# Kernel tuning notes

Hardware: AMD Instinct MI355X
Metric: run time of the kernel (lower is better)

Reference implementation:

```python
import jax, jax.numpy as jnp
import numpy as np

N = 50000
E = 1600000
IN_CH = 128
OUT_CH = 128
NEG_SLOPE = 0.2


def _gat_conv(x, W, att_src, att_dst, bias, src, dst, heads, out_ch, concat):
    # x: [N, F_in], W: [F_in, heads*out_ch], att_*: [heads, out_ch]
    n = x.shape[0]
    h = (x @ W).reshape(n, heads, out_ch)                    # [N, H, C]
    a_src = jnp.einsum('nhc,hc->nh', h, att_src)             # [N, H]
    a_dst = jnp.einsum('nhc,hc->nh', h, att_dst)             # [N, H]
    logits = jax.nn.leaky_relu(a_src[src] + a_dst[dst], NEG_SLOPE)  # [Etot, H]
    m = jax.ops.segment_max(logits, dst, num_segments=n)     # per-dst max (self-loops ensure non-empty)
    e = jnp.exp(logits - m[dst])
    denom = jax.ops.segment_sum(e, dst, num_segments=n)
    alpha = e / denom[dst]                                   # [Etot, H]
    msgs = h[src] * alpha[:, :, None]                        # [Etot, H, C]
    out = jax.ops.segment_sum(msgs, dst, num_segments=n)     # [N, H, C]
    out = out.reshape(n, heads * out_ch) if concat else out.mean(axis=1)
    return out + bias


def setup_inputs() -> dict:
    key = jax.random.key(0)
    ks = jax.random.split(key, 12)
    x = jax.random.normal(ks[0], (N, IN_CH), dtype=jnp.float32)
    edge_index = jax.random.randint(ks[1], (2, E), 0, N, dtype=jnp.int32)
    s = 0.1
    W_map = jax.random.normal(ks[2], (IN_CH, OUT_CH), dtype=jnp.float32) * s
    b_map = jnp.zeros((OUT_CH,), dtype=jnp.float32)
    # conv1: 128 -> 8 per head, 8 heads
    W1 = jax.random.normal(ks[3], (OUT_CH, 64), dtype=jnp.float32) * s
    att_src1 = jax.random.normal(ks[4], (8, 8), dtype=jnp.float32) * s
    att_dst1 = jax.random.normal(ks[5], (8, 8), dtype=jnp.float32) * s
    b1 = jnp.zeros((64,), dtype=jnp.float32)
    # conv2: 64 -> 128, 1 head, concat=False
    W2 = jax.random.normal(ks[6], (64, OUT_CH), dtype=jnp.float32) * s
    att_src2 = jax.random.normal(ks[7], (1, OUT_CH), dtype=jnp.float32) * s
    att_dst2 = jax.random.normal(ks[8], (1, OUT_CH), dtype=jnp.float32) * s
    b2 = jnp.zeros((OUT_CH,), dtype=jnp.float32)
    return {"x": x, "edge_index": edge_index, "W_map": W_map, "b_map": b_map,
            "W1": W1, "att_src1": att_src1, "att_dst1": att_dst1, "b1": b1,
            "W2": W2, "att_src2": att_src2, "att_dst2": att_dst2, "b2": b2}


def reference(x, edge_index, W_map, b_map, W1, att_src1, att_dst1, b1,
              W2, att_src2, att_dst2, b2):
    # add self-loops (PyG GATConv default)
    loops = jnp.arange(N, dtype=edge_index.dtype)
    src = jnp.concatenate([edge_index[0], loops])
    dst = jnp.concatenate([edge_index[1], loops])
    h = x @ W_map + b_map                                   # feature_mapping (dropout inactive in eval)
    h = _gat_conv(h, W1, att_src1, att_dst1, b1, src, dst, heads=8, out_ch=8, concat=True)
    h = jax.nn.elu(h)
    out = _gat_conv(h, W2, att_src2, att_dst2, b2, src, dst, heads=1, out_ch=OUT_CH, concat=False)
    return out
```

## Files before the change

kernel.cpp:

```cpp
#include <hip/hip_runtime.h>
#include <cstdint>
#include <cstddef>

#define NEG_SLOPE 0.2f
#define NBIN_MAX 1024
#define CAP_T 2560
#define SC_BLOCKS 512

typedef __attribute__((ext_vector_type(8))) short bf16x8;
typedef __attribute__((ext_vector_type(4))) float f32x4;

__device__ __forceinline__ float leaky(float x) { return x > 0.f ? x : NEG_SLOPE * x; }
__device__ __forceinline__ float blo(unsigned u) { return __uint_as_float(u << 16); }
__device__ __forceinline__ float bhi(unsigned u) { return __uint_as_float(u & 0xffff0000u); }
__device__ __forceinline__ unsigned short f2b(float f) {
    unsigned b = __float_as_uint(f);
    return (unsigned short)((b + 0x7fffu + ((b >> 16) & 1u)) >> 16);
}

__global__ void prep_kernel(const float* __restrict__ Wm, const float* __restrict__ W1,
                            const float* __restrict__ bm, const float* __restrict__ W2,
                            unsigned short* __restrict__ WcT, float* __restrict__ bc,
                            unsigned short* __restrict__ W2T, int* __restrict__ ccur,
                            int nbin) {
    int t = blockIdx.x * 256 + threadIdx.x;
    if (t < nbin) ccur[t] = 0;
    if (t < 8192) {
        int n = t >> 7, k = t & 127;
        float acc = 0.f;
        for (int c = 0; c < 128; c++) acc = fmaf(Wm[k * 128 + c], W1[c * 64 + n], acc);
        WcT[n * 128 + k] = f2b(acc);
        if (t < 64) {
            float a = 0.f;
            for (int c = 0; c < 128; c++) a = fmaf(bm[c], W1[c * 64 + t], a);
            bc[t] = a;
        }
    } else if (t < 16384) {
        int u = t - 8192;
        int n = u >> 6, k = u & 63;
        W2T[n * 64 + k] = f2b(W2[k * 128 + n]);
    }
}

__global__ __launch_bounds__(256) void phase2_kernel(
    const int* __restrict__ src, const int* __restrict__ dst, int E, int nbin,
    int* __restrict__ ccur, unsigned* __restrict__ tmp,
    const float* __restrict__ x, const unsigned short* __restrict__ WcT,
    const float* __restrict__ bc, const float* __restrict__ att_s,
    const float* __restrict__ att_d, unsigned short* __restrict__ h1b,
    float* __restrict__ as1, float* __restrict__ ad1, int N) {
    __shared__ int cnt[NBIN_MAX];
    if (blockIdx.x < SC_BLOCKS) {
        for (int i = threadIdx.x; i < nbin; i += 256) cnt[i] = 0;
        __syncthreads();
        int E4 = E >> 2;
        int chunk4 = (E4 + SC_BLOCKS - 1) / SC_BLOCKS;
        int b4 = blockIdx.x * chunk4;
        int e4 = b4 + chunk4; if (e4 > E4) e4 = E4;
        const int4* dst4 = (const int4*)dst;
        const int4* src4 = (const int4*)src;
        bool last = (blockIdx.x == SC_BLOCKS - 1);
        for (int i = b4 + threadIdx.x; i < e4; i += 256) {
            int4 d = dst4[i];
            atomicAdd(&cnt[d.x >> 6], 1);
            atomicAdd(&cnt[d.y >> 6], 1);
            atomicAdd(&cnt[d.z >> 6], 1);
            atomicAdd(&cnt[d.w >> 6], 1);
        }
        if (last)
            for (int i = (E4 << 2) + threadIdx.x; i < E; i += 256)
                atomicAdd(&cnt[dst[i] >> 6], 1);
        __syncthreads();
        for (int i = threadIdx.x; i < nbin; i += 256) {
            int c = cnt[i];
            cnt[i] = c ? atomicAdd(&ccur[i], c) : 0;
        }
        __syncthreads();
        for (int i = b4 + threadIdx.x; i < e4; i += 256) {
            int4 d = dst4[i];
            int4 s = src4[i];
#pragma unroll
            for (int k = 0; k < 4; k++) {
                int dd = (k == 0) ? d.x : (k == 1) ? d.y : (k == 2) ? d.z : d.w;
                int ss = (k == 0) ? s.x : (k == 1) ? s.y : (k == 2) ? s.z : s.w;
                int bin = dd >> 6;
                int p = atomicAdd(&cnt[bin], 1);
                if (p < CAP_T)
                    tmp[(size_t)bin * CAP_T + p] = ((unsigned)ss << 6) | (unsigned)(dd & 63);
            }
        }
        if (last)
            for (int i = (E4 << 2) + threadIdx.x; i < E; i += 256) {
                int dd = dst[i];
                int bin = dd >> 6;
                int p = atomicAdd(&cnt[bin], 1);
                if (p < CAP_T)
                    tmp[(size_t)bin * CAP_T + p] = ((unsigned)src[i] << 6) | (unsigned)(dd & 63);
            }
        return;
    }
    int wave = threadIdx.x >> 6, l = threadIdx.x & 63;
    int mtile = (blockIdx.x - SC_BLOCKS) * 4 + wave;
    int mtiles = N >> 4;
    if (mtile >= mtiles) return;
    int lm = l & 15, quad = l >> 4;
    const float* xr = x + ((size_t)(mtile * 16 + lm)) * 128 + quad * 8;
    f32x4 acc[4];
#pragma unroll
    for (int nt = 0; nt < 4; nt++) acc[nt] = (f32x4){0.f, 0.f, 0.f, 0.f};
#pragma unroll
    for (int kk = 0; kk < 4; kk++) {
        float4 xa = ((const float4*)(xr + kk * 32))[0];
        float4 xb = ((const float4*)(xr + kk * 32 + 4))[0];
        bf16x8 a;
        a[0] = (short)f2b(xa.x); a[1] = (short)f2b(xa.y);
        a[2] = (short)f2b(xa.z); a[3] = (short)f2b(xa.w);
        a[4] = (short)f2b(xb.x); a[5] = (short)f2b(xb.y);
        a[6] = (short)f2b(xb.z); a[7] = (short)f2b(xb.w);
#pragma unroll
        for (int nt = 0; nt < 4; nt++) {
            bf16x8 b = *(const bf16x8*)(WcT + (nt * 16 + lm) * 128 + kk * 32 + quad * 8);
            acc[nt] = __builtin_amdgcn_mfma_f32_16x16x32_bf16(a, b, acc[nt], 0, 0, 0);
        }
    }
    float vs[4][4], vd[4][4];
#pragma unroll
    for (int nt = 0; nt < 4; nt++) {
        int col = nt * 16 + lm;
        float sA = att_s[col], dA = att_d[col], bcv = bc[col];
#pragma unroll
        for (int r = 0; r < 4; r++) {
            float hv = acc[nt][r] + bcv;
            int row = mtile * 16 + quad * 4 + r;
            h1b[(size_t)row * 64 + col] = f2b(hv);
            vs[nt][r] = hv * sA;
            vd[nt][r] = hv * dA;
        }
    }
#pragma unroll
    for (int m = 1; m < 8; m <<= 1)
#pragma unroll
        for (int nt = 0; nt < 4; nt++)
#pragma unroll
            for (int r = 0; r < 4; r++) {
                vs[nt][r] += __shfl_xor(vs[nt][r], m);
                vd[nt][r] += __shfl_xor(vd[nt][r], m);
            }
    if ((lm & 7) == 0) {
        int hbase = lm >> 3;
#pragma unroll
        for (int nt = 0; nt < 4; nt++) {
            int H = 2 * nt + hbase;
#pragma unroll
            for (int r = 0; r < 4; r++) {
                int row = mtile * 16 + quad * 4 + r;
                as1[row * 8 + H] = vs[nt][r];
                ad1[row * 8 + H] = vd[nt][r];
            }
        }
    }
}

__global__ __launch_bounds__(256) void bin_finalize(
    const unsigned* __restrict__ tmp, const int* __restrict__ ccur,
    int* __restrict__ off, int* __restrict__ degv,
    unsigned short* __restrict__ bucket, int N) {
    __shared__ int cnt[64];
    __shared__ int cur[64];
    __shared__ unsigned short lbkt[CAP_T];
    int tid = threadIdx.x, b = blockIdx.x;
    if (tid < 64) cnt[tid] = 0;
    __syncthreads();
    int ecnt = ccur[b]; if (ecnt > CAP_T) ecnt = CAP_T;
    const unsigned* t = tmp + (size_t)b * CAP_T;
    const uint4* t4 = (const uint4*)t;
    int e4 = ecnt >> 2;
    for (int i = tid; i < e4; i += 256) {
        uint4 v = t4[i];
        atomicAdd(&cnt[v.x & 63u], 1);
        atomicAdd(&cnt[v.y & 63u], 1);
        atomicAdd(&cnt[v.z & 63u], 1);
        atomicAdd(&cnt[v.w & 63u], 1);
    }
    for (int i = (e4 << 2) + tid; i < ecnt; i += 256)
        atomicAdd(&cnt[t[i] & 63u], 1);
    __syncthreads();
    if (tid < 64) {
        int v = cnt[tid];
        int incl = v;
#pragma unroll
        for (int s = 1; s < 64; s <<= 1) {
            int u = __shfl_up(incl, s);
            if (tid >= s) incl += u;
        }
        int excl = incl - v;
        int node = b * 64 + tid;
        if (node < N) { off[node] = b * CAP_T + excl; degv[node] = v; }
        cur[tid] = excl;
    }
    __syncthreads();
    for (int i = tid; i < e4; i += 256) {
        uint4 v = t4[i];
        int p0 = atomicAdd(&cur[v.x & 63u], 1); lbkt[p0] = (unsigned short)(v.x >> 6);
        int p1 = atomicAdd(&cur[v.y & 63u], 1); lbkt[p1] = (unsigned short)(v.y >> 6);
        int p2 = atomicAdd(&cur[v.z & 63u], 1); lbkt[p2] = (unsigned short)(v.z >> 6);
        int p3 = atomicAdd(&cur[v.w & 63u], 1); lbkt[p3] = (unsigned short)(v.w >> 6);
    }
    for (int i = (e4 << 2) + tid; i < ecnt; i += 256) {
        unsigned u = t[i];
        int p = atomicAdd(&cur[u & 63u], 1);
        lbkt[p] = (unsigned short)(u >> 6);
    }
    __syncthreads();
    unsigned short* db = bucket + (size_t)b * CAP_T;
    int e8 = ecnt >> 3;
    uint4* d4 = (uint4*)db;
    const uint4* l4 = (const uint4*)lbkt;
    for (int i = tid; i < e8; i += 256) d4[i] = l4[i];
    for (int i = (e8 << 3) + tid; i < ecnt; i += 256) db[i] = lbkt[i];
}

__global__ __launch_bounds__(256) void conv1_agg(
    const int* __restrict__ off, const int* __restrict__ degv,
    const unsigned short* __restrict__ bucket,
    const unsigned* __restrict__ h1b, const float* __restrict__ as1,
    const float* __restrict__ ad1, const float* __restrict__ b1,
    unsigned* __restrict__ h1act, int N) {
    int wave = threadIdx.x >> 6, l = threadIdx.x & 63;
    int n = blockIdx.x * 4 + wave;
    if (n >= N) return;
    int begin = off[n];
    int deg = degv[n];
    int oo = l & 7, octet = l >> 3;
    unsigned qoff = (unsigned)(oo << 4);
    const char* h1c = (const char*)h1b;
    float adst = ad1[n * 8 + oo];
    float wself = __expf(leaky(as1[n * 8 + oo] + adst));
    float acc[8] = {0.f, 0.f, 0.f, 0.f, 0.f, 0.f, 0.f, 0.f};
    if (octet == 0) {
        uint4 us = *(const uint4*)(h1c + ((size_t)n << 7) + qoff);
        acc[0] = wself * blo(us.x); acc[1] = wself * bhi(us.x);
        acc[2] = wself * blo(us.y); acc[3] = wself * bhi(us.y);
        acc[4] = wself * blo(us.z); acc[5] = wself * bhi(us.z);
        acc[6] = wself * blo(us.w); acc[7] = wself * bhi(us.w);
    }
    float den_l = 0.f;
    unsigned sv[8]; float av[8];
#pragma unroll
    for (int j = 0; j < 8; j++) {
        int e = 8 * j + octet;
        unsigned sraw = (unsigned)bucket[begin + e];
        sv[j] = (e < deg) ? sraw : 0u;
    }
#pragma unroll
    for (int j = 0; j < 8; j++) {
        float t = as1[sv[j] * 8 + oo];
        av[j] = (8 * j + octet < deg) ? t : -1e30f;
    }
    for (int c0 = 0; c0 < deg; c0 += 64) {
        uint4 uv[8];
#pragma unroll
        for (int j = 0; j < 8; j++)
            uv[j] = *(const uint4*)(h1c + ((size_t)sv[j] << 7) + qoff);
        int c1 = c0 + 64;
        bool more = c1 < deg;
        unsigned sn[8];
        if (more) {
#pragma unroll
            for (int j = 0; j < 8; j++) {
                int e = c1 + 8 * j + octet;
                unsigned sraw = (unsigned)bucket[begin + e];
                sn[j] = (e < deg) ? sraw : 0u;
            }
        }
        float wv[8];
#pragma unroll
        for (int j = 0; j < 8; j++) {
            float w = __expf(leaky(av[j] + adst));
            wv[j] = w; den_l += w;
        }
        if (more) {
#pragma unroll
            for (int j = 0; j < 8; j++) {
                float t = as1[sn[j] * 8 + oo];
                av[j] = (c1 + 8 * j + octet < deg) ? t : -1e30f;
                sv[j] = sn[j];
            }
        }
#pragma unroll
        for (int j = 0; j < 8; j++) {
            acc[0] = fmaf(wv[j], blo(uv[j].x), acc[0]);
            acc[1] = fmaf(wv[j], bhi(uv[j].x), acc[1]);
            acc[2] = fmaf(wv[j], blo(uv[j].y), acc[2]);
            acc[3] = fmaf(wv[j], bhi(uv[j].y), acc[3]);
            acc[4] = fmaf(wv[j], blo(uv[j].z), acc[4]);
            acc[5] = fmaf(wv[j], bhi(uv[j].z), acc[5]);
            acc[6] = fmaf(wv[j], blo(uv[j].w), acc[6]);
            acc[7] = fmaf(wv[j], bhi(uv[j].w), acc[7]);
        }
    }
    den_l += __shfl_xor(den_l, 8);
    den_l += __shfl_xor(den_l, 16);
    den_l += __shfl_xor(den_l, 32);
    float den = den_l + wself;
#pragma unroll
    for (int i = 0; i < 8; i++) {
        acc[i] += __shfl_xor(acc[i], 8);
        acc[i] += __shfl_xor(acc[i], 16);
        acc[i] += __shfl_xor(acc[i], 32);
    }
    if (octet == 0) {
        float inv = 1.f / den;
        float4 b0 = ((const float4*)b1)[oo * 2];
        float4 b1v = ((const float4*)b1)[oo * 2 + 1];
        float o0 = acc[0] * inv + b0.x;
        float o1 = acc[1] * inv + b0.y;
        float o2 = acc[2] * inv + b0.z;
        float o3 = acc[3] * inv + b0.w;
        float o4 = acc[4] * inv + b1v.x;
        float o5 = acc[5] * inv + b1v.y;
        float o6 = acc[6] * inv + b1v.z;
        float o7 = acc[7] * inv + b1v.w;
        o0 = o0 > 0.f ? o0 : __expf(o0) - 1.f;
        o1 = o1 > 0.f ? o1 : __expf(o1) - 1.f;
        o2 = o2 > 0.f ? o2 : __expf(o2) - 1.f;
        o3 = o3 > 0.f ? o3 : __expf(o3) - 1.f;
        o4 = o4 > 0.f ? o4 : __expf(o4) - 1.f;
        o5 = o5 > 0.f ? o5 : __expf(o5) - 1.f;
        o6 = o6 > 0.f ? o6 : __expf(o6) - 1.f;
        o7 = o7 > 0.f ? o7 : __expf(o7) - 1.f;
        unsigned r0 = (unsigned)f2b(o0) | ((unsigned)f2b(o1) << 16);
        unsigned r1 = (unsigned)f2b(o2) | ((unsigned)f2b(o3) << 16);
        unsigned r2 = (unsigned)f2b(o4) | ((unsigned)f2b(o5) << 16);
        unsigned r3 = (unsigned)f2b(o6) | ((unsigned)f2b(o7) << 16);
        ((uint4*)h1act)[(size_t)n * 8 + oo] = make_uint4(r0, r1, r2, r3);
    }
}

__global__ __launch_bounds__(256) void gemm2_mfma(
    const unsigned short* __restrict__ h1act, const unsigned short* __restrict__ W2T,
    const float* __restrict__ att_s2, const float* __restrict__ att_d2,
    unsigned short* __restrict__ h2b, float* __restrict__ as2, float* __restrict__ ad2,
    int N) {
    int wave = threadIdx.x >> 6, l = threadIdx.x & 63;
    int mtile = blockIdx.x * 4 + wave;
    int mtiles = N >> 4;
    if (mtile >= mtiles) return;
    int lm = l & 15, quad = l >> 4;
    const unsigned short* ar = h1act + (size_t)(mtile * 16 + lm) * 64 + quad * 8;
    bf16x8 a0 = *(const bf16x8*)(ar);
    bf16x8 a1 = *(const bf16x8*)(ar + 32);
    f32x4 acc[8];
#pragma unroll
    for (int nt = 0; nt < 8; nt++) acc[nt] = (f32x4){0.f, 0.f, 0.f, 0.f};
#pragma unroll
    for (int nt = 0; nt < 8; nt++) {
        const unsigned short* br = W2T + (nt * 16 + lm) * 64 + quad * 8;
        bf16x8 b0 = *(const bf16x8*)(br);
        bf16x8 b1v = *(const bf16x8*)(br + 32);
        acc[nt] = __builtin_amdgcn_mfma_f32_16x16x32_bf16(a0, b0, acc[nt], 0, 0, 0);
        acc[nt] = __builtin_amdgcn_mfma_f32_16x16x32_bf16(a1, b1v, acc[nt], 0, 0, 0);
    }
    float vs[4] = {0.f, 0.f, 0.f, 0.f}, vd[4] = {0.f, 0.f, 0.f, 0.f};
#pragma unroll
    for (int nt = 0; nt < 8; nt++) {
        int col = nt * 16 + lm;
        float sA = att_s2[col], dA = att_d2[col];
#pragma unroll
        for (int r = 0; r < 4; r++) {
            float hv = acc[nt][r];
            int row = mtile * 16 + quad * 4 + r;
            h2b[(size_t)row * 128 + col] = f2b(hv);
            vs[r] = fmaf(hv, sA, vs[r]);
            vd[r] = fmaf(hv, dA, vd[r]);
        }
    }
#pragma unroll
    for (int m = 1; m < 16; m <<= 1)
#pragma unroll
        for (int r = 0; r < 4; r++) {
            vs[r] += __shfl_xor(vs[r], m);
            vd[r] += __shfl_xor(vd[r], m);
        }
    if (lm == 0) {
#pragma unroll
        for (int r = 0; r < 4; r++) {
            int row = mtile * 16 + quad * 4 + r;
            as2[row] = vs[r];
            ad2[row] = vd[r];
        }
    }
}

__global__ __launch_bounds__(256) void conv2_agg(
    const int* __restrict__ off, const int* __restrict__ degv,
    const unsigned short* __restrict__ bucket,
    const unsigned* __restrict__ h2b, const float* __restrict__ as2,
    const float* __restrict__ ad2, const float* __restrict__ b2,
    float* __restrict__ out, int N) {
    __shared__ uint2 ew[4][64];
    int wave = threadIdx.x >> 6, l = threadIdx.x & 63;
    int n = blockIdx.x * 4 + wave;
    if (n >= N) return;
    int begin = off[n];
    int deg = degv[n];
    int qq = l & 15, quarter = l >> 4;
    unsigned qoff = (unsigned)(qq << 4);
    const char* h2c = (const char*)h2b;
    float adst = ad2[n];
    float wself = __expf(leaky(as2[n] + adst));
    float acc[8] = {0.f, 0.f, 0.f, 0.f, 0.f, 0.f, 0.f, 0.f};
    if (quarter == 0) {
        uint4 us = *(const uint4*)(h2c + ((size_t)n << 8) + qoff);
        acc[0] = wself * blo(us.x); acc[1] = wself * bhi(us.x);
        acc[2] = wself * blo(us.y); acc[3] = wself * bhi(us.y);
        acc[4] = wself * blo(us.z); acc[5] = wself * bhi(us.z);
        acc[6] = wself * blo(us.w); acc[7] = wself * bhi(us.w);
    }
    uint2 wA[4], wB[4];
    uint4 uA[4], uB[4];
    auto loadg = [&](uint2 (&pw)[4], uint4 (&uv)[4], int g) {
#pragma unroll
        for (int k = 0; k < 4; k++) {
            pw[k] = ew[wave][16 * g + 4 * k + quarter];
            uv[k] = *(const uint4*)(h2c + pw[k].y + qoff);
        }
    };
    auto fmag = [&](uint2 (&pw)[4], uint4 (&uv)[4]) {
#pragma unroll
        for (int k = 0; k < 4; k++) {
            float w_ = __uint_as_float(pw[k].x);
            acc[0] = fmaf(w_, blo(uv[k].x), acc[0]);
            acc[1] = fmaf(w_, bhi(uv[k].x), acc[1]);
            acc[2] = fmaf(w_, blo(uv[k].y), acc[2]);
            acc[3] = fmaf(w_, bhi(uv[k].y), acc[3]);
            acc[4] = fmaf(w_, blo(uv[k].z), acc[4]);
            acc[5] = fmaf(w_, bhi(uv[k].z), acc[5]);
            acc[6] = fmaf(w_, blo(uv[k].w), acc[6]);
            acc[7] = fmaf(w_, bhi(uv[k].w), acc[7]);
        }
    };
    float den_l = 0.f;
    for (int c0 = 0; c0 < deg; c0 += 64) {
        int j = c0 + l;
        unsigned sraw = (unsigned)bucket[begin + j];
        unsigned s = (j < deg) ? sraw : 0u;
        float a = as2[s];
        a = (j < deg) ? a : -1e30f;
        float w = __expf(leaky(a + adst));
        den_l += w;
        ew[wave][l] = make_uint2(__float_as_uint(w), s << 8);
        int cend = deg - c0; if (cend > 64) cend = 64;
        int ng = (cend + 15) >> 4;
        loadg(wA, uA, 0);
        int g = 1;
        for (; g + 1 < ng; g += 2) {
            loadg(wB, uB, g);
            fmag(wA, uA);
            loadg(wA, uA, g + 1);
            fmag(wB, uB);
        }
        if (g < ng) {
            loadg(wB, uB, g);
            fmag(wA, uA);
            fmag(wB, uB);
        } else {
            fmag(wA, uA);
        }
    }
#pragma unroll
    for (int s = 1; s < 64; s <<= 1) den_l += __shfl_xor(den_l, s);
    float den = den_l + wself;
#pragma unroll
    for (int i = 0; i < 8; i++) {
        acc[i] += __shfl_xor(acc[i], 16);
        acc[i] += __shfl_xor(acc[i], 32);
    }
    if (quarter == 0) {
        float inv = 1.f / den;
        float4 b0 = ((const float4*)b2)[qq * 2];
        float4 b1v = ((const float4*)b2)[qq * 2 + 1];
        ((float4*)out)[(size_t)n * 32 + qq * 2] = make_float4(
            acc[0] * inv + b0.x, acc[1] * inv + b0.y,
            acc[2] * inv + b0.z, acc[3] * inv + b0.w);
        ((float4*)out)[(size_t)n * 32 + qq * 2 + 1] = make_float4(
            acc[4] * inv + b1v.x, acc[5] * inv + b1v.y,
            acc[6] * inv + b1v.z, acc[7] * inv + b1v.w);
    }
}

extern "C" void kernel_launch(void* const* d_in, const int* in_sizes, int n_in,
                              void* d_out, int out_size, void* d_ws, size_t ws_size,
                              hipStream_t stream) {
    const float* x   = (const float*)d_in[0];
    const int*   ei  = (const int*)d_in[1];
    const float* Wm  = (const float*)d_in[2];
    const float* bm  = (const float*)d_in[3];
    const float* W1  = (const float*)d_in[4];
    const float* As1 = (const float*)d_in[5];
    const float* Ad1 = (const float*)d_in[6];
    const float* b1  = (const float*)d_in[7];
    const float* W2  = (const float*)d_in[8];
    const float* As2 = (const float*)d_in[9];
    const float* Ad2 = (const float*)d_in[10];
    const float* b2  = (const float*)d_in[11];
    int N = in_sizes[0] / 128;
    int E = in_sizes[1] / 2;
    const int* srcv = ei;
    const int* dstv = ei + E;

    char* p = (char*)d_ws;
    auto alloc = [&](size_t bytes) {
        void* r = (void*)p;
        p += (bytes + 255) & ~(size_t)255;
        return r;
    };
    int nbin = (N + 63) / 64;
    int*   degv   = (int*)alloc((size_t)N * 4);
    int*   off    = (int*)alloc((size_t)N * 4);
    int*   ccur   = (int*)alloc((size_t)nbin * 4);
    unsigned short* bucket = (unsigned short*)alloc((size_t)nbin * CAP_T * 2);
    unsigned short* WcT  = (unsigned short*)alloc(64 * 128 * 2);
    float*          bc   = (float*)alloc(64 * 4);
    unsigned short* W2T  = (unsigned short*)alloc(128 * 64 * 2);
    unsigned short* h1b  = (unsigned short*)alloc((size_t)N * 64 * 2);
    float* a_s1   = (float*)alloc((size_t)N * 8 * 4);
    float* a_d1   = (float*)alloc((size_t)N * 8 * 4);
    unsigned* h1act = (unsigned*)alloc((size_t)N * 64 * 2);
    unsigned short* h2b = (unsigned short*)alloc((size_t)N * 128 * 2);
    unsigned* tmp = (unsigned*)h2b;
    float* a_s2   = (float*)alloc((size_t)N * 4);
    float* a_d2   = (float*)alloc((size_t)N * 4);
    float* outp   = (float*)d_out;

    int mtiles = N >> 4;
    int gemm_blocks = (mtiles + 3) / 4;
    prep_kernel<<<64, 256, 0, stream>>>(Wm, W1, bm, W2, WcT, bc, W2T, ccur, nbin);
    phase2_kernel<<<SC_BLOCKS + gemm_blocks, 256, 0, stream>>>(
        srcv, dstv, E, nbin, ccur, tmp, x, WcT, bc, As1, Ad1, h1b, a_s1, a_d1, N);
    bin_finalize<<<nbin, 256, 0, stream>>>(tmp, ccur, off, degv, bucket, N);
    conv1_agg<<<(N + 3) / 4, 256, 0, stream>>>(off, degv, bucket, (const unsigned*)h1b, a_s1, a_d1, b1, h1act, N);
    gemm2_mfma<<<(mtiles + 3) / 4, 256, 0, stream>>>((const unsigned short*)h1act, W2T, As2, Ad2, h2b, a_s2, a_d2, N);
    conv2_agg<<<(N + 3) / 4, 256, 0, stream>>>(off, degv, bucket, (const unsigned*)h2b, a_s2, a_d2, b2, outp, N);
}
```

Measured before the change: 270.2 us.

## Replace two-level binned CSR build with global count, scan and scatter

The two-pass shared-memory binning into fixed-capacity 64-node bins, followed by a per-bin finalize kernel, is replaced by a standard CSR build. A count kernel does global atomic degree counting, a single-block kernel scans the degrees into offsets, and a scatter phase writes source ids through global atomic cursors. This removes the temporary buffer, the finalize pass and the per-bin capacity cap. In exchange it adds two kernel launches, a serial one-block scan over 50k nodes, and roughly 3.2M scattered global atomics with 2-byte scattered writes in place of shared-memory atomics.

```diff
diff --git a/kernel.cpp b/kernel.cpp
--- a/kernel.cpp
+++ b/kernel.cpp
@@ -3,8 +3,6 @@
 #include <cstddef>
 
 #define NEG_SLOPE 0.2f
-#define NBIN_MAX 1024
-#define CAP_T 2560
 #define SC_BLOCKS 512
 
 typedef __attribute__((ext_vector_type(8))) short bf16x8;
@@ -21,10 +19,10 @@
 __global__ void prep_kernel(const float* __restrict__ Wm, const float* __restrict__ W1,
                             const float* __restrict__ bm, const float* __restrict__ W2,
                             unsigned short* __restrict__ WcT, float* __restrict__ bc,
-                            unsigned short* __restrict__ W2T, int* __restrict__ ccur,
-                            int nbin) {
+                            unsigned short* __restrict__ W2T, int* __restrict__ degv,
+                            int N) {
     int t = blockIdx.x * 256 + threadIdx.x;
-    if (t < nbin) ccur[t] = 0;
+    for (int i = t; i < N; i += 16384) degv[i] = 0;
     if (t < 8192) {
         int n = t >> 7, k = t & 127;
         float acc = 0.f;
@@ -42,60 +40,85 @@
     }
 }
 
+__global__ __launch_bounds__(256) void count_kernel(const int* __restrict__ dst, int E,
+                                                    int* __restrict__ degv) {
+    int E4 = E >> 2;
+    const int4* d4 = (const int4*)dst;
+    int stride = gridDim.x * 256;
+    for (int i = blockIdx.x * 256 + threadIdx.x; i < E4; i += stride) {
+        int4 d = d4[i];
+        atomicAdd(&degv[d.x], 1);
+        atomicAdd(&degv[d.y], 1);
+        atomicAdd(&degv[d.z], 1);
+        atomicAdd(&degv[d.w], 1);
+    }
+    if (blockIdx.x == 0)
+        for (int i = (E4 << 2) + threadIdx.x; i < E; i += 256)
+            atomicAdd(&degv[dst[i]], 1);
+}
+
+__global__ __launch_bounds__(1024) void scan_kernel(const int* __restrict__ degv,
+                                                    int* __restrict__ off,
+                                                    int* __restrict__ cursor, int N) {
+    __shared__ int wsum[16];
+    __shared__ int carry_s;
+    int tid = threadIdx.x, w = tid >> 6, l = tid & 63;
+    if (tid == 0) carry_s = 0;
+    __syncthreads();
+    for (int base = 0; base < N; base += 1024) {
+        int i = base + tid;
+        int v = (i < N) ? degv[i] : 0;
+        int incl = v;
+#pragma unroll
+        for (int s = 1; s < 64; s <<= 1) {
+            int u = __shfl_up(incl, s);
+            if (l >= s) incl += u;
+        }
+        if (l == 63) wsum[w] = incl;
+        __syncthreads();
+        if (tid < 16) {
+            int x = wsum[tid];
+#pragma unroll
+            for (int s = 1; s < 16; s <<= 1) {
+                int u = __shfl_up(x, s);
+                if (tid >= s) x += u;
+            }
+            wsum[tid] = x;
+        }
+        __syncthreads();
+        int carry = carry_s;
+        int excl = incl - v + (w ? wsum[w - 1] : 0) + carry;
+        if (i < N) { off[i] = excl; cursor[i] = excl; }
+        __syncthreads();
+        if (tid == 0) carry_s = carry + wsum[15];
+        __syncthreads();
+    }
+}
+
 __global__ __launch_bounds__(256) void phase2_kernel(
-    const int* __restrict__ src, const int* __restrict__ dst, int E, int nbin,
-    int* __restrict__ ccur, unsigned* __restrict__ tmp,
+    const int* __restrict__ src, const int* __restrict__ dst, int E,
+    int* __restrict__ cursor, unsigned short* __restrict__ bucket,
     const float* __restrict__ x, const unsigned short* __restrict__ WcT,
     const float* __restrict__ bc, const float* __restrict__ att_s,
     const float* __restrict__ att_d, unsigned short* __restrict__ h1b,
     float* __restrict__ as1, float* __restrict__ ad1, int N) {
-    __shared__ int cnt[NBIN_MAX];
     if (blockIdx.x < SC_BLOCKS) {
-        for (int i = threadIdx.x; i < nbin; i += 256) cnt[i] = 0;
-        __syncthreads();
         int E4 = E >> 2;
-        int chunk4 = (E4 + SC_BLOCKS - 1) / SC_BLOCKS;
-        int b4 = blockIdx.x * chunk4;
-        int e4 = b4 + chunk4; if (e4 > E4) e4 = E4;
         const int4* dst4 = (const int4*)dst;
         const int4* src4 = (const int4*)src;
-        bool last = (blockIdx.x == SC_BLOCKS - 1);
-        for (int i = b4 + threadIdx.x; i < e4; i += 256) {
-            int4 d = dst4[i];
-            atomicAdd(&cnt[d.x >> 6], 1);
-            atomicAdd(&cnt[d.y >> 6], 1);
-            atomicAdd(&cnt[d.z >> 6], 1);
-            atomicAdd(&cnt[d.w >> 6], 1);
-        }
-        if (last)
-            for (int i = (E4 << 2) + threadIdx.x; i < E; i += 256)
-                atomicAdd(&cnt[dst[i] >> 6], 1);
-        __syncthreads();
-        for (int i = threadIdx.x; i < nbin; i += 256) {
-            int c = cnt[i];
-            cnt[i] = c ? atomicAdd(&ccur[i], c) : 0;
-        }
-        __syncthreads();
-        for (int i = b4 + threadIdx.x; i < e4; i += 256) {
+        int stride = SC_BLOCKS * 256;
+        for (int i = blockIdx.x * 256 + threadIdx.x; i < E4; i += stride) {
             int4 d = dst4[i];
             int4 s = src4[i];
-#pragma unroll
-            for (int k = 0; k < 4; k++) {
-                int dd = (k == 0) ? d.x : (k == 1) ? d.y : (k == 2) ? d.z : d.w;
-                int ss = (k == 0) ? s.x : (k == 1) ? s.y : (k == 2) ? s.z : s.w;
-                int bin = dd >> 6;
-                int p = atomicAdd(&cnt[bin], 1);
-                if (p < CAP_T)
-                    tmp[(size_t)bin * CAP_T + p] = ((unsigned)ss << 6) | (unsigned)(dd & 63);
-            }
-        }
-        if (last)
+            int p0 = atomicAdd(&cursor[d.x], 1); bucket[p0] = (unsigned short)s.x;
+            int p1 = atomicAdd(&cursor[d.y], 1); bucket[p1] = (unsigned short)s.y;
+            int p2 = atomicAdd(&cursor[d.z], 1); bucket[p2] = (unsigned short)s.z;
+            int p3 = atomicAdd(&cursor[d.w], 1); bucket[p3] = (unsigned short)s.w;
+        }
+        if (blockIdx.x == 0)
             for (int i = (E4 << 2) + threadIdx.x; i < E; i += 256) {
-                int dd = dst[i];
-                int bin = dd >> 6;
-                int p = atomicAdd(&cnt[bin], 1);
-                if (p < CAP_T)
-                    tmp[(size_t)bin * CAP_T + p] = ((unsigned)src[i] << 6) | (unsigned)(dd & 63);
+                int p = atomicAdd(&cursor[dst[i]], 1);
+                bucket[p] = (unsigned short)src[i];
             }
         return;
     }
@@ -159,65 +182,6 @@
             }
         }
     }
-}
-
-__global__ __launch_bounds__(256) void bin_finalize(
-    const unsigned* __restrict__ tmp, const int* __restrict__ ccur,
-    int* __restrict__ off, int* __restrict__ degv,
-    unsigned short* __restrict__ bucket, int N) {
-    __shared__ int cnt[64];
-    __shared__ int cur[64];
-    __shared__ unsigned short lbkt[CAP_T];
-    int tid = threadIdx.x, b = blockIdx.x;
-    if (tid < 64) cnt[tid] = 0;
-    __syncthreads();
-    int ecnt = ccur[b]; if (ecnt > CAP_T) ecnt = CAP_T;
-    const unsigned* t = tmp + (size_t)b * CAP_T;
-    const uint4* t4 = (const uint4*)t;
-    int e4 = ecnt >> 2;
-    for (int i = tid; i < e4; i += 256) {
-        uint4 v = t4[i];
-        atomicAdd(&cnt[v.x & 63u], 1);
-        atomicAdd(&cnt[v.y & 63u], 1);
-        atomicAdd(&cnt[v.z & 63u], 1);
-        atomicAdd(&cnt[v.w & 63u], 1);
-    }
-    for (int i = (e4 << 2) + tid; i < ecnt; i += 256)
-        atomicAdd(&cnt[t[i] & 63u], 1);
-    __syncthreads();
-    if (tid < 64) {
-        int v = cnt[tid];
-        int incl = v;
-#pragma unroll
-        for (int s = 1; s < 64; s <<= 1) {
-            int u = __shfl_up(incl, s);
-            if (tid >= s) incl += u;
-        }
-        int excl = incl - v;
-        int node = b * 64 + tid;
-        if (node < N) { off[node] = b * CAP_T + excl; degv[node] = v; }
-        cur[tid] = excl;
-    }
-    __syncthreads();
-    for (int i = tid; i < e4; i += 256) {
-        uint4 v = t4[i];
-        int p0 = atomicAdd(&cur[v.x & 63u], 1); lbkt[p0] = (unsigned short)(v.x >> 6);
-        int p1 = atomicAdd(&cur[v.y & 63u], 1); lbkt[p1] = (unsigned short)(v.y >> 6);
-        int p2 = atomicAdd(&cur[v.z & 63u], 1); lbkt[p2] = (unsigned short)(v.z >> 6);
-        int p3 = atomicAdd(&cur[v.w & 63u], 1); lbkt[p3] = (unsigned short)(v.w >> 6);
-    }
-    for (int i = (e4 << 2) + tid; i < ecnt; i += 256) {
-        unsigned u = t[i];
-        int p = atomicAdd(&cur[u & 63u], 1);
-        lbkt[p] = (unsigned short)(u >> 6);
-    }
-    __syncthreads();
-    unsigned short* db = bucket + (size_t)b * CAP_T;
-    int e8 = ecnt >> 3;
-    uint4* d4 = (uint4*)db;
-    const uint4* l4 = (const uint4*)lbkt;
-    for (int i = tid; i < e8; i += 256) d4[i] = l4[i];
-    for (int i = (e8 << 3) + tid; i < ecnt; i += 256) db[i] = lbkt[i];
 }
 
 __global__ __launch_bounds__(256) void conv1_agg(
@@ -515,11 +479,10 @@
         p += (bytes + 255) & ~(size_t)255;
         return r;
     };
-    int nbin = (N + 63) / 64;
     int*   degv   = (int*)alloc((size_t)N * 4);
     int*   off    = (int*)alloc((size_t)N * 4);
-    int*   ccur   = (int*)alloc((size_t)nbin * 4);
-    unsigned short* bucket = (unsigned short*)alloc((size_t)nbin * CAP_T * 2);
+    int*   cursor = (int*)alloc((size_t)N * 4);
+    unsigned short* bucket = (unsigned short*)alloc(((size_t)E + 128) * 2);
     unsigned short* WcT  = (unsigned short*)alloc(64 * 128 * 2);
     float*          bc   = (float*)alloc(64 * 4);
     unsigned short* W2T  = (unsigned short*)alloc(128 * 64 * 2);
@@ -528,17 +491,17 @@
     float* a_d1   = (float*)alloc((size_t)N * 8 * 4);
     unsigned* h1act = (unsigned*)alloc((size_t)N * 64 * 2);
     unsigned short* h2b = (unsigned short*)alloc((size_t)N * 128 * 2);
-    unsigned* tmp = (unsigned*)h2b;
     float* a_s2   = (float*)alloc((size_t)N * 4);
     float* a_d2   = (float*)alloc((size_t)N * 4);
     float* outp   = (float*)d_out;
 
     int mtiles = N >> 4;
     int gemm_blocks = (mtiles + 3) / 4;
-    prep_kernel<<<64, 256, 0, stream>>>(Wm, W1, bm, W2, WcT, bc, W2T, ccur, nbin);
+    prep_kernel<<<64, 256, 0, stream>>>(Wm, W1, bm, W2, WcT, bc, W2T, degv, N);
+    count_kernel<<<512, 256, 0, stream>>>(dstv, E, degv);
+    scan_kernel<<<1, 1024, 0, stream>>>(degv, off, cursor, N);
     phase2_kernel<<<SC_BLOCKS + gemm_blocks, 256, 0, stream>>>(
-        srcv, dstv, E, nbin, ccur, tmp, x, WcT, bc, As1, Ad1, h1b, a_s1, a_d1, N);
-    bin_finalize<<<nbin, 256, 0, stream>>>(tmp, ccur, off, degv, bucket, N);
+        srcv, dstv, E, cursor, bucket, x, WcT, bc, As1, Ad1, h1b, a_s1, a_d1, N);
     conv1_agg<<<(N + 3) / 4, 256, 0, stream>>>(off, degv, bucket, (const unsigned*)h1b, a_s1, a_d1, b1, h1act, N);
     gemm2_mfma<<<(mtiles + 3) / 4, 256, 0, stream>>>((const unsigned short*)h1act, W2T, As2, Ad2, h2b, a_s2, a_d2, N);
     conv2_agg<<<(N + 3) / 4, 256, 0, stream>>>(off, degv, bucket, (const unsigned*)h2b, a_s2, a_d2, b2, outp, N);
```

After: 429.9 us. 59.1% more time.
